# Performance work log

Measured on AMD Instinct MI355X. Metric: run time of the kernel, lower is better.

The kernel has to match this reference:

```python
import jax, jax.numpy as jnp
import numpy as np

D = 64        # emb_size
L = 4         # n_layers
ND = 4        # directions per layer: v2c, c2v, v2k, k2v
N_VAR, N_CONS, N_CUT = 100000, 50000, 20000
E_VC, E_VK = 800000, 200000
EF = 8        # edge feature dim
LN_EPS = 1e-3  # keras LayerNormalization default epsilon


def mlp2(x, w1, b1, w2, b2):
    # Dense(relu) -> Dense(linear); dropout is identity (training=False)
    return jax.nn.relu(x @ w1 + b1) @ w2 + b2


def layer_norm(x, g, b):
    m = jnp.mean(x, axis=-1, keepdims=True)
    v = jnp.var(x, axis=-1, keepdims=True)
    return (x - m) * jax.lax.rsqrt(v + LN_EPS) * g + b


def message_pass(node, neigh, src, dst, ew, P, i):
    """One MessagePassingLayer. P is a tuple of stacked [16,...] params, i the layer index."""
    (mw1, mb1, mw2, mb2, gw, gb, uw1, ub1, uw2, ub2, lg, lb) = P
    msg = mlp2(neigh, mw1[i], mb1[i], mw2[i], mb2[i])          # [N_src, D]
    wm = msg[src] * ew                                          # [E, D] gather + weight
    n = node.shape[0]
    agg = jax.ops.segment_sum(wm, dst, num_segments=n)          # scatter_nd sum
    deg = jax.ops.segment_sum(ew, dst, num_segments=n)          # [n, 1]
    agg = agg / jnp.maximum(deg, 1.0)
    comb = jnp.concatenate([agg, node], axis=-1)                # [n, 2D]
    gate = jax.nn.sigmoid(comb @ gw[i] + gb[i])
    upd = mlp2(comb, uw1[i], ub1[i], uw2[i], ub2[i])
    out = gate * upd + (1.0 - gate) * node
    return layer_norm(out, lg[i], lb[i])


def edge_weight(src_f, dst_f, e_f, w1, b1, w2, b2):
    comb = jnp.concatenate([src_f, dst_f, e_f], axis=-1)
    return jax.nn.sigmoid(jax.nn.relu(comb @ w1 + b1) @ w2 + b2)  # [E, 1]


def setup_inputs() -> dict:
    keys = iter(jax.random.split(jax.random.key(0), 64))

    def p(shape, scale=0.05):
        return jax.random.normal(next(keys), shape, dtype=jnp.float32) * scale

    inp = {
        'variable_features': jax.random.normal(next(keys), (N_VAR, 19), dtype=jnp.float32),
        'constraint_features': jax.random.normal(next(keys), (N_CONS, 5), dtype=jnp.float32),
        'cut_features': jax.random.normal(next(keys), (N_CUT, 30), dtype=jnp.float32),
        'var_cons_edge_features': jax.random.normal(next(keys), (E_VC, EF), dtype=jnp.float32),
        'var_cut_edge_features': jax.random.normal(next(keys), (E_VK, EF), dtype=jnp.float32),
        'var_cons_edges': jnp.stack([
            jax.random.randint(next(keys), (E_VC,), 0, N_VAR, dtype=jnp.int32),
            jax.random.randint(next(keys), (E_VC,), 0, N_CONS, dtype=jnp.int32)]),
        'var_cut_edges': jnp.stack([
            jax.random.randint(next(keys), (E_VK,), 0, N_VAR, dtype=jnp.int32),
            jax.random.randint(next(keys), (E_VK,), 0, N_CUT, dtype=jnp.int32)]),
    }
    # embedding MLPs
    for name, din in [('var', 19), ('cons', 5), ('cut', 30)]:
        inp[f'{name}_w1'] = p((din, D)); inp[f'{name}_b1'] = p((D,))
        inp[f'{name}_w2'] = p((D, D));  inp[f'{name}_b2'] = p((D,))
    # edge weight modules (input 2D + edge_feat)
    for name in ['ewvc', 'ewvk']:
        inp[f'{name}_w1'] = p((2 * D + EF, D)); inp[f'{name}_b1'] = p((D,))
        inp[f'{name}_w2'] = p((D, 1));          inp[f'{name}_b2'] = p((1,))
    # 16 message passing layers, stacked; index = layer*4 + direction(v2c,c2v,v2k,k2v)
    NL = L * ND
    inp['mp_msg_w1'] = p((NL, D, D));  inp['mp_msg_b1'] = p((NL, D))
    inp['mp_msg_w2'] = p((NL, D, D));  inp['mp_msg_b2'] = p((NL, D))
    inp['mp_gate_w'] = p((NL, 2 * D, D)); inp['mp_gate_b'] = p((NL, D))
    inp['mp_upd_w1'] = p((NL, 2 * D, D)); inp['mp_upd_b1'] = p((NL, D))
    inp['mp_upd_w2'] = p((NL, D, D));  inp['mp_upd_b2'] = p((NL, D))
    inp['mp_ln_g'] = jnp.ones((NL, D), dtype=jnp.float32)
    inp['mp_ln_b'] = jnp.zeros((NL, D), dtype=jnp.float32)
    return inp


def reference(variable_features, constraint_features, cut_features,
              var_cons_edge_features, var_cut_edge_features,
              var_w1, var_b1, var_w2, var_b2,
              cons_w1, cons_b1, cons_w2, cons_b2,
              cut_w1, cut_b1, cut_w2, cut_b2,
              ewvc_w1, ewvc_b1, ewvc_w2, ewvc_b2,
              ewvk_w1, ewvk_b1, ewvk_w2, ewvk_b2,
              mp_msg_w1, mp_msg_b1, mp_msg_w2, mp_msg_b2,
              mp_gate_w, mp_gate_b, mp_upd_w1, mp_upd_b1,
              mp_upd_w2, mp_upd_b2, mp_ln_g, mp_ln_b,
              var_cons_edges, var_cut_edges):
    h_var = mlp2(variable_features, var_w1, var_b1, var_w2, var_b2)
    h_cons = mlp2(constraint_features, cons_w1, cons_b1, cons_w2, cons_b2)
    h_cut = mlp2(cut_features, cut_w1, cut_b1, cut_w2, cut_b2)

    vc_s, vc_d = var_cons_edges[0], var_cons_edges[1]
    vk_s, vk_d = var_cut_edges[0], var_cut_edges[1]

    vc_w = edge_weight(h_var[vc_s], h_cons[vc_d], var_cons_edge_features,
                       ewvc_w1, ewvc_b1, ewvc_w2, ewvc_b2)
    vk_w = edge_weight(h_var[vk_s], h_cut[vk_d], var_cut_edge_features,
                       ewvk_w1, ewvk_b1, ewvk_w2, ewvk_b2)

    P = (mp_msg_w1, mp_msg_b1, mp_msg_w2, mp_msg_b2, mp_gate_w, mp_gate_b,
         mp_upd_w1, mp_upd_b1, mp_upd_w2, mp_upd_b2, mp_ln_g, mp_ln_b)

    for l in range(L):
        h_cons = message_pass(h_cons, h_var, vc_s, vc_d, vc_w, P, l * ND + 0)
        h_var = message_pass(h_var, h_cons, vc_d, vc_s, vc_w, P, l * ND + 1)  # reverse
        h_cut = message_pass(h_cut, h_var, vk_s, vk_d, vk_w, P, l * ND + 2)
        h_var = message_pass(h_var, h_cut, vk_d, vk_s, vk_w, P, l * ND + 3)  # reverse
    return h_cut
```

## Files before the change

kernel.cpp:

```cpp
#include <hip/hip_runtime.h>

#define DEVINL static __device__ __forceinline__

namespace {

typedef __attribute__((ext_vector_type(8))) short bf16x8;
typedef __attribute__((ext_vector_type(4))) float f32x4;

constexpr int NV = 100000;
constexpr int NC = 50000;
constexpr int NK = 20000;
constexpr int EVC = 800000;
constexpr int EVK = 200000;
constexpr int E_TOT2 = 2 * (EVC + EVK);
constexpr int R_TOT = NC + NV + NK + NV;
constexpr int SCAN_CHUNK = 2048;
constexpr int SCAN_NB = (R_TOT + SCAN_CHUNK - 1) / SCAN_CHUNK;
constexpr int PACK_PER_LAYER = 28672;
constexpr float WQ_SCALE = 16383.0f;
constexpr float WQ_INV = 1.0f / 16383.0f;

__constant__ int c_bin_hi[8] = {12500, 25000, 37500, 50000,
                                83334, 116667, 150000, 270000};
__constant__ int c_seg_lo[8] = {0, 0, 0, 0, EVC, EVC, EVC, 2 * EVC};
__constant__ int c_seg_hi[8] = {EVC, EVC, EVC, EVC,
                                2 * EVC, 2 * EVC, 2 * EVC, E_TOT2};

constexpr int PE_VAR_W1 = 0;
constexpr int PE_VAR_W2 = 2048;
constexpr int PE_CONS_W1 = 6144;
constexpr int PE_CONS_W2 = 8192;
constexpr int PE_CUT_W1 = 12288;
constexpr int PE_CUT_W2 = 14336;
constexpr int PE_EWVC_A = 18432;
constexpr int PE_EWVC_B = 22528;
constexpr int PE_EWVK_A = 26624;
constexpr int PE_EWVK_B = 30720;
constexpr int PE_TOTAL = 34816;

DEVINL unsigned short f2bf(float f) {
  unsigned u = __float_as_uint(f);
  u = u + 0x7fffu + ((u >> 16) & 1u);
  return (unsigned short)(u >> 16);
}
DEVINL float bf2f(unsigned short h) {
  return __uint_as_float((unsigned)h << 16);
}

DEVINL float sigmoid_f(float x) { return 1.0f / (1.0f + __expf(-x)); }

DEVINL void pack_mat(const float* __restrict__ src, int K, int Kpad,
                     unsigned short* __restrict__ dst, int tid) {
  const int ntup = (Kpad / 32) * 256;
  for (int tup = tid; tup < ntup; tup += 256) {
    const int lane = tup & 63;
    const int t = (tup >> 6) & 3;
    const int kb = tup >> 8;
    const int c = t * 16 + (lane & 15);
    const int k0 = kb * 32 + (lane >> 4) * 8;
#pragma unroll
    for (int jj = 0; jj < 8; ++jj)
      dst[tup * 8 + jj] =
          (k0 + jj < K) ? f2bf(src[(k0 + jj) * 64 + c]) : (unsigned short)0;
  }
}

__global__ void __launch_bounds__(256) pack_k(
    const float* __restrict__ mW1, const float* __restrict__ mW2,
    const float* __restrict__ gW, const float* __restrict__ uW1,
    const float* __restrict__ uW2, unsigned short* __restrict__ PW) {
  const int layer = blockIdx.x;
  unsigned short* out = PW + (size_t)layer * PACK_PER_LAYER;
  pack_mat(mW1 + (size_t)layer * 4096, 64, 64, out, threadIdx.x);
  pack_mat(mW2 + (size_t)layer * 4096, 64, 64, out + 4096, threadIdx.x);
  pack_mat(gW + (size_t)layer * 8192, 128, 128, out + 8192, threadIdx.x);
  pack_mat(uW1 + (size_t)layer * 8192, 128, 128, out + 16384, threadIdx.x);
  pack_mat(uW2 + (size_t)layer * 4096, 64, 64, out + 24576, threadIdx.x);
}

__global__ void __launch_bounds__(256) pack_emb_k(
    const float* __restrict__ var_w1, const float* __restrict__ var_w2,
    const float* __restrict__ cons_w1, const float* __restrict__ cons_w2,
    const float* __restrict__ cut_w1, const float* __restrict__ cut_w2,
    const float* __restrict__ ewvc_w1, const float* __restrict__ ewvk_w1,
    unsigned short* __restrict__ P) {
  switch (blockIdx.x) {
    case 0: pack_mat(var_w1, 19, 32, P + PE_VAR_W1, threadIdx.x); break;
    case 1: pack_mat(var_w2, 64, 64, P + PE_VAR_W2, threadIdx.x); break;
    case 2: pack_mat(cons_w1, 5, 32, P + PE_CONS_W1, threadIdx.x); break;
    case 3: pack_mat(cons_w2, 64, 64, P + PE_CONS_W2, threadIdx.x); break;
    case 4: pack_mat(cut_w1, 30, 32, P + PE_CUT_W1, threadIdx.x); break;
    case 5: pack_mat(cut_w2, 64, 64, P + PE_CUT_W2, threadIdx.x); break;
    case 6: pack_mat(ewvc_w1, 64, 64, P + PE_EWVC_A, threadIdx.x); break;
    case 7: pack_mat(ewvc_w1 + 64 * 64, 64, 64, P + PE_EWVC_B, threadIdx.x); break;
    case 8: pack_mat(ewvk_w1, 64, 64, P + PE_EWVK_A, threadIdx.x); break;
    case 9: pack_mat(ewvk_w1 + 64 * 64, 64, 64, P + PE_EWVK_B, threadIdx.x); break;
  }
}

template <int DIN>
__global__ void __launch_bounds__(256) emb_mfma_k(
    const float* __restrict__ X, const unsigned short* __restrict__ W1p_,
    const unsigned short* __restrict__ W2p_, const float* __restrict__ B1,
    const float* __restrict__ B2, unsigned short* __restrict__ OUTb, int N) {
  __shared__ unsigned short lds[4][16 * 72];
  const int wave = threadIdx.x >> 6, l = threadIdx.x & 63;
  const int col = l & 15, quad = l >> 4;
  const int n0_raw = blockIdx.x * 64 + wave * 16;
  const bool dead = n0_raw >= N;
  const int n0 = dead ? 0 : n0_raw;

  bf16x8 a0;
#pragma unroll
  for (int j = 0; j < 8; ++j) {
    const int k = quad * 8 + j;
    a0[j] = (k < DIN) ? (short)f2bf(X[(size_t)(n0 + col) * DIN + k]) : (short)0;
  }
  const bf16x8* W1p = (const bf16x8*)W1p_;
  const bf16x8* W2p = (const bf16x8*)W2p_;
  f32x4 acc[4];
#pragma unroll
  for (int t = 0; t < 4; ++t) {
    const float b = B1[col + 16 * t];
    acc[t] = f32x4{b, b, b, b};
  }
#pragma unroll
  for (int t = 0; t < 4; ++t)
    acc[t] = __builtin_amdgcn_mfma_f32_16x16x32_bf16(a0, W1p[t * 64 + l], acc[t], 0, 0, 0);
  unsigned short* ld = lds[wave];
#pragma unroll
  for (int t = 0; t < 4; ++t)
#pragma unroll
    for (int r = 0; r < 4; ++r)
      ld[(quad * 4 + r) * 72 + col + 16 * t] = f2bf(fmaxf(acc[t][r], 0.0f));
  __syncthreads();
  const bf16x8 h0 = *(const bf16x8*)&ld[col * 72 + quad * 8];
  const bf16x8 h1 = *(const bf16x8*)&ld[col * 72 + 32 + quad * 8];
  f32x4 o[4];
#pragma unroll
  for (int t = 0; t < 4; ++t) {
    const float b = B2[col + 16 * t];
    o[t] = f32x4{b, b, b, b};
  }
#pragma unroll
  for (int t = 0; t < 4; ++t) {
    o[t] = __builtin_amdgcn_mfma_f32_16x16x32_bf16(h0, W2p[t * 64 + l], o[t], 0, 0, 0);
    o[t] = __builtin_amdgcn_mfma_f32_16x16x32_bf16(h1, W2p[(4 + t) * 64 + l], o[t], 0, 0, 0);
  }
  __syncthreads();
#pragma unroll
  for (int t = 0; t < 4; ++t)
#pragma unroll
    for (int r = 0; r < 4; ++r)
      ld[(quad * 4 + r) * 72 + col + 16 * t] = f2bf(o[t][r]);
  __syncthreads();
  if (!dead) {
#pragma unroll
    for (int cc = 0; cc < 2; ++cc) {
      const bf16x8 v = *(const bf16x8*)&ld[col * 72 + (quad * 2 + cc) * 8];
      *(bf16x8*)(OUTb + (size_t)(n0 + col) * 64 + (quad * 2 + cc) * 8) = v;
    }
  }
}

template <int NOUT>
__global__ void __launch_bounds__(256) gemv_mfma_k(
    const unsigned short* __restrict__ Xb, const unsigned short* __restrict__ WpA_,
    const unsigned short* __restrict__ WpB_, const float* __restrict__ Bias,
    unsigned short* __restrict__ OUT0, unsigned short* __restrict__ OUT1, int N) {
  __shared__ unsigned short lds[4][16 * 72];
  const int wave = threadIdx.x >> 6, l = threadIdx.x & 63;
  const int col = l & 15, quad = l >> 4;
  const int n0_raw = blockIdx.x * 64 + wave * 16;
  const bool dead = n0_raw >= N;
  const int n0 = dead ? 0 : n0_raw;
  const unsigned short* xrow = Xb + (size_t)(n0 + col) * 64 + quad * 8;
  const bf16x8 a0 = *(const bf16x8*)xrow;
  const bf16x8 a1 = *(const bf16x8*)(xrow + 32);
  unsigned short* ld = lds[wave];
#pragma unroll
  for (int m = 0; m < NOUT; ++m) {
    const bf16x8* Wp = (const bf16x8*)(m == 0 ? WpA_ : WpB_);
    unsigned short* OUT = (m == 0) ? OUT0 : OUT1;
    f32x4 acc[4];
#pragma unroll
    for (int t = 0; t < 4; ++t) {
      const float b = (Bias != nullptr) ? Bias[col + 16 * t] : 0.0f;
      acc[t] = f32x4{b, b, b, b};
    }
#pragma unroll
    for (int t = 0; t < 4; ++t) {
      acc[t] = __builtin_amdgcn_mfma_f32_16x16x32_bf16(a0, Wp[t * 64 + l], acc[t], 0, 0, 0);
      acc[t] = __builtin_amdgcn_mfma_f32_16x16x32_bf16(a1, Wp[(4 + t) * 64 + l], acc[t], 0, 0, 0);
    }
    if (m > 0) __syncthreads();
#pragma unroll
    for (int t = 0; t < 4; ++t)
#pragma unroll
      for (int r = 0; r < 4; ++r)
        ld[(quad * 4 + r) * 72 + col + 16 * t] = f2bf(acc[t][r]);
    __syncthreads();
    if (!dead) {
#pragma unroll
      for (int cc = 0; cc < 2; ++cc) {
        const bf16x8 v = *(const bf16x8*)&ld[col * 72 + (quad * 2 + cc) * 8];
        *(bf16x8*)(OUT + (size_t)(n0 + col) * 64 + (quad * 2 + cc) * 8) = v;
      }
    }
  }
}

__global__ void __launch_bounds__(256) msg_mfma_k(
    const unsigned short* __restrict__ Xb, const unsigned short* __restrict__ Wp,
    const float* __restrict__ B1, const float* __restrict__ B2,
    unsigned short* __restrict__ MSGb, int N) {
  __shared__ unsigned short lds[4][16 * 72];
  const int wave = threadIdx.x >> 6, l = threadIdx.x & 63;
  const int col = l & 15, quad = l >> 4;
  const int n0_raw = blockIdx.x * 64 + wave * 16;
  const bool dead = n0_raw >= N;
  const int n0 = dead ? 0 : n0_raw;

  const unsigned short* xrow = Xb + (size_t)(n0 + col) * 64 + quad * 8;
  const bf16x8 a0 = *(const bf16x8*)xrow;
  const bf16x8 a1 = *(const bf16x8*)(xrow + 32);
  const bf16x8* W1p = (const bf16x8*)Wp;
  const bf16x8* W2p = (const bf16x8*)(Wp + 4096);

  f32x4 acc[4];
#pragma unroll
  for (int t = 0; t < 4; ++t) {
    const float b = B1[col + 16 * t];
    acc[t] = f32x4{b, b, b, b};
  }
#pragma unroll
  for (int t = 0; t < 4; ++t) {
    acc[t] = __builtin_amdgcn_mfma_f32_16x16x32_bf16(a0, W1p[t * 64 + l], acc[t], 0, 0, 0);
    acc[t] = __builtin_amdgcn_mfma_f32_16x16x32_bf16(a1, W1p[(4 + t) * 64 + l], acc[t], 0, 0, 0);
  }
  unsigned short* ld = lds[wave];
#pragma unroll
  for (int t = 0; t < 4; ++t)
#pragma unroll
    for (int r = 0; r < 4; ++r)
      ld[(quad * 4 + r) * 72 + col + 16 * t] = f2bf(fmaxf(acc[t][r], 0.0f));
  __syncthreads();
  const bf16x8 h0 = *(const bf16x8*)&ld[col * 72 + quad * 8];
  const bf16x8 h1 = *(const bf16x8*)&ld[col * 72 + 32 + quad * 8];
  f32x4 o[4];
#pragma unroll
  for (int t = 0; t < 4; ++t) {
    const float b = B2[col + 16 * t];
    o[t] = f32x4{b, b, b, b};
  }
#pragma unroll
  for (int t = 0; t < 4; ++t) {
    o[t] = __builtin_amdgcn_mfma_f32_16x16x32_bf16(h0, W2p[t * 64 + l], o[t], 0, 0, 0);
    o[t] = __builtin_amdgcn_mfma_f32_16x16x32_bf16(h1, W2p[(4 + t) * 64 + l], o[t], 0, 0, 0);
  }
  __syncthreads();
#pragma unroll
  for (int t = 0; t < 4; ++t)
#pragma unroll
    for (int r = 0; r < 4; ++r)
      ld[(quad * 4 + r) * 72 + col + 16 * t] = f2bf(o[t][r]);
  __syncthreads();
  if (!dead) {
#pragma unroll
    for (int cc = 0; cc < 2; ++cc) {
      const bf16x8 v = *(const bf16x8*)&ld[col * 72 + (quad * 2 + cc) * 8];
      *(bf16x8*)(MSGb + (size_t)(n0 + col) * 64 + (quad * 2 + cc) * 8) = v;
    }
  }
}

template <int WITH_MSG>
__global__ void __launch_bounds__(256) pass_mfma_k(
    const int* __restrict__ row_ptr, const unsigned* __restrict__ adj,
    const float* __restrict__ degi, const unsigned short* __restrict__ MSGsrc,
    const unsigned short* __restrict__ NODEb,
    const unsigned short* __restrict__ gWp, const unsigned short* __restrict__ uW1p,
    const unsigned short* __restrict__ uW2p, const float* __restrict__ gB,
    const float* __restrict__ uB1, const float* __restrict__ uB2,
    const float* __restrict__ LNG, const float* __restrict__ LNB,
    const unsigned short* __restrict__ mWp,
    const float* __restrict__ mB1, const float* __restrict__ mB2,
    float* __restrict__ OUTf, unsigned short* __restrict__ OUTb,
    unsigned short* __restrict__ MSGdst, int base, int N) {
  __shared__ unsigned short lds[4][16 * 72];
  const int wave = threadIdx.x >> 6, l = threadIdx.x & 63;
  const int col = l & 15, quad = l >> 4;
  const int n0_raw = blockIdx.x * 64 + wave * 16;
  const bool dead = n0_raw >= N;
  const int n0 = dead ? 0 : n0_raw;

  const int r = base + n0 + col;
  const int ps = row_ptr[r], pe = row_ptr[r + 1];
  float acc0[8], acc1[8];
#pragma unroll
  for (int j = 0; j < 8; ++j) { acc0[j] = 0.0f; acc1[j] = 0.0f; }
  int p = ps;
  for (; p + 4 <= pe; p += 4) {
    unsigned av[4];
#pragma unroll
    for (int j = 0; j < 4; ++j) av[j] = adj[p + j];
    bf16x8 m0[4], m1[4];
#pragma unroll
    for (int j = 0; j < 4; ++j) {
      const unsigned short* m = MSGsrc + (size_t)(av[j] >> 14) * 64 + quad * 8;
      m0[j] = *(const bf16x8*)m;
      m1[j] = *(const bf16x8*)(m + 32);
    }
#pragma unroll
    for (int j = 0; j < 4; ++j) {
      const float w = (float)(av[j] & 16383u) * WQ_INV;
      const unsigned* u0 = (const unsigned*)&m0[j];
      const unsigned* u1 = (const unsigned*)&m1[j];
#pragma unroll
      for (int q = 0; q < 4; ++q) {
        acc0[2 * q] = fmaf(__uint_as_float(u0[q] << 16), w, acc0[2 * q]);
        acc0[2 * q + 1] = fmaf(__uint_as_float(u0[q] & 0xffff0000u), w, acc0[2 * q + 1]);
        acc1[2 * q] = fmaf(__uint_as_float(u1[q] << 16), w, acc1[2 * q]);
        acc1[2 * q + 1] = fmaf(__uint_as_float(u1[q] & 0xffff0000u), w, acc1[2 * q + 1]);
      }
    }
  }
  for (; p + 2 <= pe; p += 2) {
    const unsigned avA = adj[p], avB = adj[p + 1];
    const unsigned short* mA = MSGsrc + (size_t)(avA >> 14) * 64 + quad * 8;
    const unsigned short* mB = MSGsrc + (size_t)(avB >> 14) * 64 + quad * 8;
    const bf16x8 mA0 = *(const bf16x8*)mA;
    const bf16x8 mA1 = *(const bf16x8*)(mA + 32);
    const bf16x8 mB0 = *(const bf16x8*)mB;
    const bf16x8 mB1v = *(const bf16x8*)(mB + 32);
    const float wA = (float)(avA & 16383u) * WQ_INV;
    const float wB = (float)(avB & 16383u) * WQ_INV;
    const unsigned* uA0 = (const unsigned*)&mA0;
    const unsigned* uA1 = (const unsigned*)&mA1;
    const unsigned* uB0 = (const unsigned*)&mB0;
    const unsigned* uB1v = (const unsigned*)&mB1v;
#pragma unroll
    for (int q = 0; q < 4; ++q) {
      acc0[2 * q] = fmaf(__uint_as_float(uA0[q] << 16), wA, acc0[2 * q]);
      acc0[2 * q + 1] = fmaf(__uint_as_float(uA0[q] & 0xffff0000u), wA, acc0[2 * q + 1]);
      acc1[2 * q] = fmaf(__uint_as_float(uA1[q] << 16), wA, acc1[2 * q]);
      acc1[2 * q + 1] = fmaf(__uint_as_float(uA1[q] & 0xffff0000u), wA, acc1[2 * q + 1]);
      acc0[2 * q] = fmaf(__uint_as_float(uB0[q] << 16), wB, acc0[2 * q]);
      acc0[2 * q + 1] = fmaf(__uint_as_float(uB0[q] & 0xffff0000u), wB, acc0[2 * q + 1]);
      acc1[2 * q] = fmaf(__uint_as_float(uB1v[q] << 16), wB, acc1[2 * q]);
      acc1[2 * q + 1] = fmaf(__uint_as_float(uB1v[q] & 0xffff0000u), wB, acc1[2 * q + 1]);
    }
  }
  if (p < pe) {
    const unsigned av = adj[p];
    const unsigned short* m = MSGsrc + (size_t)(av >> 14) * 64 + quad * 8;
    const bf16x8 m0 = *(const bf16x8*)m;
    const bf16x8 m1 = *(const bf16x8*)(m + 32);
    const float w = (float)(av & 16383u) * WQ_INV;
    const unsigned* u0 = (const unsigned*)&m0;
    const unsigned* u1 = (const unsigned*)&m1;
#pragma unroll
    for (int q = 0; q < 4; ++q) {
      acc0[2 * q] = fmaf(__uint_as_float(u0[q] << 16), w, acc0[2 * q]);
      acc0[2 * q + 1] = fmaf(__uint_as_float(u0[q] & 0xffff0000u), w, acc0[2 * q + 1]);
      acc1[2 * q] = fmaf(__uint_as_float(u1[q] << 16), w, acc1[2 * q]);
      acc1[2 * q + 1] = fmaf(__uint_as_float(u1[q] & 0xffff0000u), w, acc1[2 * q + 1]);
    }
  }
  const float di = degi[r];
  bf16x8 aA0, aA1;
#pragma unroll
  for (int j = 0; j < 8; ++j) {
    aA0[j] = (short)f2bf(acc0[j] * di);
    aA1[j] = (short)f2bf(acc1[j] * di);
  }

  const unsigned short* nrow = NODEb + (size_t)(n0 + col) * 64 + quad * 8;
  const bf16x8 aN0 = *(const bf16x8*)nrow;
  const bf16x8 aN1 = *(const bf16x8*)(nrow + 32);
  const bf16x8* gW = (const bf16x8*)gWp;
  const bf16x8* uW1 = (const bf16x8*)uW1p;
  const bf16x8* uW2 = (const bf16x8*)uW2p;

  f32x4 g[4], u[4];
#pragma unroll
  for (int t = 0; t < 4; ++t) {
    const float bg = gB[col + 16 * t], bu = uB1[col + 16 * t];
    g[t] = f32x4{bg, bg, bg, bg};
    u[t] = f32x4{bu, bu, bu, bu};
  }
#pragma unroll
  for (int t = 0; t < 4; ++t) {
    g[t] = __builtin_amdgcn_mfma_f32_16x16x32_bf16(aA0, gW[t * 64 + l], g[t], 0, 0, 0);
    g[t] = __builtin_amdgcn_mfma_f32_16x16x32_bf16(aA1, gW[(4 + t) * 64 + l], g[t], 0, 0, 0);
    g[t] = __builtin_amdgcn_mfma_f32_16x16x32_bf16(aN0, gW[(8 + t) * 64 + l], g[t], 0, 0, 0);
    g[t] = __builtin_amdgcn_mfma_f32_16x16x32_bf16(aN1, gW[(12 + t) * 64 + l], g[t], 0, 0, 0);
    u[t] = __builtin_amdgcn_mfma_f32_16x16x32_bf16(aA0, uW1[t * 64 + l], u[t], 0, 0, 0);
    u[t] = __builtin_amdgcn_mfma_f32_16x16x32_bf16(aA1, uW1[(4 + t) * 64 + l], u[t], 0, 0, 0);
    u[t] = __builtin_amdgcn_mfma_f32_16x16x32_bf16(aN0, uW1[(8 + t) * 64 + l], u[t], 0, 0, 0);
    u[t] = __builtin_amdgcn_mfma_f32_16x16x32_bf16(aN1, uW1[(12 + t) * 64 + l], u[t], 0, 0, 0);
  }
#pragma unroll
  for (int t = 0; t < 4; ++t)
#pragma unroll
    for (int r2 = 0; r2 < 4; ++r2) g[t][r2] = sigmoid_f(g[t][r2]);

  unsigned short* ld = lds[wave];
#pragma unroll
  for (int t = 0; t < 4; ++t)
#pragma unroll
    for (int r2 = 0; r2 < 4; ++r2)
      ld[(quad * 4 + r2) * 72 + col + 16 * t] = f2bf(fmaxf(u[t][r2], 0.0f));
  const bf16x8 h0 = *(const bf16x8*)&ld[col * 72 + quad * 8];
  const bf16x8 h1 = *(const bf16x8*)&ld[col * 72 + 32 + quad * 8];
  f32x4 o[4];
#pragma unroll
  for (int t = 0; t < 4; ++t) {
    const float b = uB2[col + 16 * t];
    o[t] = f32x4{b, b, b, b};
  }
#pragma unroll
  for (int t = 0; t < 4; ++t) {
    o[t] = __builtin_amdgcn_mfma_f32_16x16x32_bf16(h0, uW2[t * 64 + l], o[t], 0, 0, 0);
    o[t] = __builtin_amdgcn_mfma_f32_16x16x32_bf16(h1, uW2[(4 + t) * 64 + l], o[t], 0, 0, 0);
  }
  float om[4][4];
#pragma unroll
  for (int t = 0; t < 4; ++t)
#pragma unroll
    for (int r2 = 0; r2 < 4; ++r2) {
      const float nd =
          bf2f(NODEb[(size_t)(n0 + quad * 4 + r2) * 64 + col + 16 * t]);
      om[t][r2] = fmaf(g[t][r2], o[t][r2] - nd, nd);
    }
  float outv[4][4];
#pragma unroll
  for (int r2 = 0; r2 < 4; ++r2) {
    float s1 = (om[0][r2] + om[1][r2]) + (om[2][r2] + om[3][r2]);
    float s2 = fmaf(om[0][r2], om[0][r2], fmaf(om[1][r2], om[1][r2],
                fmaf(om[2][r2], om[2][r2], om[3][r2] * om[3][r2])));
#pragma unroll
    for (int off = 1; off < 16; off <<= 1) {
      s1 += __shfl_xor(s1, off, 64);
      s2 += __shfl_xor(s2, off, 64);
    }
    const float m = s1 * (1.0f / 64.0f);
    const float var = s2 * (1.0f / 64.0f) - m * m;
    const float rr = rsqrtf(var + 1e-3f);
#pragma unroll
    for (int t = 0; t < 4; ++t)
      outv[t][r2] = fmaf((om[t][r2] - m) * rr, LNG[col + 16 * t], LNB[col + 16 * t]);
  }
  if (OUTf != nullptr && !dead) {
#pragma unroll
    for (int t = 0; t < 4; ++t)
#pragma unroll
      for (int r2 = 0; r2 < 4; ++r2)
        OUTf[(size_t)(n0 + quad * 4 + r2) * 64 + col + 16 * t] = outv[t][r2];
  }
#pragma unroll
  for (int t = 0; t < 4; ++t)
#pragma unroll
    for (int r2 = 0; r2 < 4; ++r2)
      ld[(quad * 4 + r2) * 72 + col + 16 * t] = f2bf(outv[t][r2]);
  if (OUTb != nullptr && !dead) {
#pragma unroll
    for (int cc = 0; cc < 2; ++cc) {
      const bf16x8 v = *(const bf16x8*)&ld[col * 72 + (quad * 2 + cc) * 8];
      *(bf16x8*)(OUTb + (size_t)(n0 + col) * 64 + (quad * 2 + cc) * 8) = v;
    }
  }

  if constexpr (WITH_MSG) {
    const bf16x8 x0 = *(const bf16x8*)&ld[col * 72 + quad * 8];
    const bf16x8 x1 = *(const bf16x8*)&ld[col * 72 + 32 + quad * 8];
    const bf16x8* W1p = (const bf16x8*)mWp;
    const bf16x8* W2p = (const bf16x8*)(mWp + 4096);
    f32x4 macc[4];
#pragma unroll
    for (int t = 0; t < 4; ++t) {
      const float b = mB1[col + 16 * t];
      macc[t] = f32x4{b, b, b, b};
    }
#pragma unroll
    for (int t = 0; t < 4; ++t) {
      macc[t] = __builtin_amdgcn_mfma_f32_16x16x32_bf16(x0, W1p[t * 64 + l], macc[t], 0, 0, 0);
      macc[t] = __builtin_amdgcn_mfma_f32_16x16x32_bf16(x1, W1p[(4 + t) * 64 + l], macc[t], 0, 0, 0);
    }
#pragma unroll
    for (int t = 0; t < 4; ++t)
#pragma unroll
      for (int r2 = 0; r2 < 4; ++r2)
        ld[(quad * 4 + r2) * 72 + col + 16 * t] = f2bf(fmaxf(macc[t][r2], 0.0f));
    const bf16x8 mh0 = *(const bf16x8*)&ld[col * 72 + quad * 8];
    const bf16x8 mh1 = *(const bf16x8*)&ld[col * 72 + 32 + quad * 8];
    f32x4 mo[4];
#pragma unroll
    for (int t = 0; t < 4; ++t) {
      const float b = mB2[col + 16 * t];
      mo[t] = f32x4{b, b, b, b};
    }
#pragma unroll
    for (int t = 0; t < 4; ++t) {
      mo[t] = __builtin_amdgcn_mfma_f32_16x16x32_bf16(mh0, W2p[t * 64 + l], mo[t], 0, 0, 0);
      mo[t] = __builtin_amdgcn_mfma_f32_16x16x32_bf16(mh1, W2p[(4 + t) * 64 + l], mo[t], 0, 0, 0);
    }
#pragma unroll
    for (int t = 0; t < 4; ++t)
#pragma unroll
      for (int r2 = 0; r2 < 4; ++r2)
        ld[(quad * 4 + r2) * 72 + col + 16 * t] = f2bf(mo[t][r2]);
    if (!dead) {
#pragma unroll
      for (int cc = 0; cc < 2; ++cc) {
        const bf16x8 v = *(const bf16x8*)&ld[col * 72 + (quad * 2 + cc) * 8];
        *(bf16x8*)(MSGdst + (size_t)(n0 + col) * 64 + (quad * 2 + cc) * 8) = v;
      }
    }
  }
}

__global__ void __launch_bounds__(256) edgew_k(
    const int* __restrict__ S, const int* __restrict__ D,
    const float* __restrict__ EFX, const unsigned short* __restrict__ PA,
    const unsigned short* __restrict__ PB, const float* __restrict__ W1C,
    const float* __restrict__ W2, const float* __restrict__ B2,
    unsigned long long* __restrict__ stagedD,
    unsigned long long* __restrict__ stagedS,
    int* __restrict__ counts, int baseD, int baseS, int E) {
  const int l = threadIdx.x & 63;
  const int g = l >> 3, c = l & 7;
  float wc[8][8];
#pragma unroll
  for (int i = 0; i < 8; ++i) {
    const float4 v0 = *(const float4*)(W1C + i * 64 + c * 8);
    const float4 v1 = *(const float4*)(W1C + i * 64 + c * 8 + 4);
    wc[i][0] = v0.x; wc[i][1] = v0.y; wc[i][2] = v0.z; wc[i][3] = v0.w;
    wc[i][4] = v1.x; wc[i][5] = v1.y; wc[i][6] = v1.z; wc[i][7] = v1.w;
  }
  float w2c[8];
  {
    const float4 a0 = *(const float4*)(W2 + c * 8);
    const float4 a1 = *(const float4*)(W2 + c * 8 + 4);
    w2c[0] = a0.x; w2c[1] = a0.y; w2c[2] = a0.z; w2c[3] = a0.w;
    w2c[4] = a1.x; w2c[5] = a1.y; w2c[6] = a1.z; w2c[7] = a1.w;
  }
  const float b2 = B2[0];
  const int wave_id = blockIdx.x * 4 + (threadIdx.x >> 6);
  const int nwaves = gridDim.x * 4;
  for (int t0 = wave_id * 8; t0 < E; t0 += nwaves * 8) {
    const int e = t0 + g;
    const bool ok = e < E;
    const int ee = ok ? e : E - 1;
    const int s = __builtin_nontemporal_load(S + ee);
    const int d = __builtin_nontemporal_load(D + ee);
    int kd = 0, ks = 0;
    const int rd = baseD + d, rs = baseS + s;
    if (ok && c == 0) {
      kd = atomicAdd(&counts[rd], 1);
      ks = atomicAdd(&counts[rs], 1);
    }
    const bf16x8 pa = *(const bf16x8*)(PA + (size_t)s * 64 + c * 8);
    const bf16x8 pb = *(const bf16x8*)(PB + (size_t)d * 64 + c * 8);
    const f32x4 ef0 =
        __builtin_nontemporal_load((const f32x4*)(EFX + (size_t)ee * 8));
    const f32x4 ef1 =
        __builtin_nontemporal_load((const f32x4*)(EFX + (size_t)ee * 8 + 4));
    const unsigned* pau = (const unsigned*)&pa;
    const unsigned* pbu = (const unsigned*)&pb;
    float h[8];
#pragma unroll
    for (int q = 0; q < 4; ++q) {
      h[2 * q] = __uint_as_float(pau[q] << 16) + __uint_as_float(pbu[q] << 16);
      h[2 * q + 1] = __uint_as_float(pau[q] & 0xffff0000u) +
                     __uint_as_float(pbu[q] & 0xffff0000u);
    }
    const float ef[8] = {ef0[0], ef0[1], ef0[2], ef0[3],
                         ef1[0], ef1[1], ef1[2], ef1[3]};
#pragma unroll
    for (int i = 0; i < 8; ++i)
#pragma unroll
      for (int j = 0; j < 8; ++j) h[j] = fmaf(ef[i], wc[i][j], h[j]);
    float t = 0.0f;
#pragma unroll
    for (int j = 0; j < 8; ++j) t = fmaf(fmaxf(h[j], 0.0f), w2c[j], t);
#pragma unroll
    for (int off = 1; off < 8; off <<= 1) t += __shfl_xor(t, off, 64);
    if (ok && c == 0) {
      const float w = sigmoid_f(t + b2);
      const unsigned w14 = (unsigned)(w * WQ_SCALE + 0.5f);
      stagedD[e] =
          (unsigned long long)((unsigned)rd | ((unsigned)kd << 19)) |
          ((unsigned long long)(((unsigned)s << 14) | w14) << 32);
      stagedS[e] =
          (unsigned long long)((unsigned)rs | ((unsigned)ks << 19)) |
          ((unsigned long long)(((unsigned)d << 14) | w14) << 32);
    }
  }
}

__global__ void __launch_bounds__(256) fill_staged_k(
    const unsigned long long* __restrict__ staged,
    const int* __restrict__ row_ptr, unsigned* __restrict__ adj) {
  const int bin = blockIdx.x & 7;
  const int blk = blockIdx.x >> 3;
  const int nblk = gridDim.x >> 3;
  const int lo = (bin == 0) ? 0 : c_bin_hi[bin - 1];
  const int hi = c_bin_hi[bin];
  const int slo = c_seg_lo[bin], shi = c_seg_hi[bin];
  for (int i = slo + blk * 256 + threadIdx.x; i < shi; i += nblk * 256) {
    const unsigned long long v = __builtin_nontemporal_load(staged + i);
    const int row = (int)(v & 0x7ffffull);
    if (row >= lo && row < hi) {
      const int k = (int)((v >> 19) & 0x1fffull);
      adj[row_ptr[row] + k] = (unsigned)(v >> 32);
    }
  }
}

__global__ void __launch_bounds__(256) degi_k(const int* __restrict__ row_ptr,
                                             const unsigned* __restrict__ adj,
                                             float* __restrict__ degi) {
  const int r = blockIdx.x * 256 + threadIdx.x;
  if (r >= R_TOT) return;
  const int s = row_ptr[r], e = row_ptr[r + 1];
  float d = 0.0f;
  for (int p = s; p < e; ++p) d += (float)(adj[p] & 16383u) * WQ_INV;
  degi[r] = 1.0f / fmaxf(d, 1.0f);
}

__global__ void __launch_bounds__(256) scan1_k(const int* __restrict__ in,
                                               int* __restrict__ bsum) {
  __shared__ int sd[256];
  const int t = threadIdx.x;
  const int base = blockIdx.x * SCAN_CHUNK + t * 8;
  int s = 0;
#pragma unroll
  for (int i = 0; i < 8; ++i) {
    const int idx = base + i;
    s += (idx < R_TOT) ? in[idx] : 0;
  }
  sd[t] = s;
  __syncthreads();
  for (int off = 128; off > 0; off >>= 1) {
    if (t < off) sd[t] += sd[t + off];
    __syncthreads();
  }
  if (t == 0) bsum[blockIdx.x] = sd[0];
}

__global__ void __launch_bounds__(256) scan2_k(int* __restrict__ bsum,
                                               int* __restrict__ row_ptr) {
  __shared__ int sd[256];
  const int t = threadIdx.x;
  const int v = (t < SCAN_NB) ? bsum[t] : 0;
  sd[t] = v;
  __syncthreads();
  for (int off = 1; off < 256; off <<= 1) {
    const int add = (t >= off) ? sd[t - off] : 0;
    __syncthreads();
    sd[t] += add;
    __syncthreads();
  }
  if (t < SCAN_NB) bsum[t] = sd[t] - v;
  if (t == 255) row_ptr[R_TOT] = sd[255];
}

__global__ void __launch_bounds__(256) scan3_k(const int* __restrict__ in,
                                               const int* __restrict__ bsum,
                                               int* __restrict__ out) {
  __shared__ int sd[256];
  const int t = threadIdx.x;
  const int base = blockIdx.x * SCAN_CHUNK + t * 8;
  int loc[8];
  int s = 0;
#pragma unroll
  for (int i = 0; i < 8; ++i) {
    loc[i] = s;
    const int idx = base + i;
    s += (idx < R_TOT) ? in[idx] : 0;
  }
  sd[t] = s;
  __syncthreads();
  const int v = s;
  for (int off = 1; off < 256; off <<= 1) {
    const int add = (t >= off) ? sd[t - off] : 0;
    __syncthreads();
    sd[t] += add;
    __syncthreads();
  }
  const int off0 = bsum[blockIdx.x] + (sd[t] - v);
#pragma unroll
  for (int i = 0; i < 8; ++i) {
    const int idx = base + i;
    if (idx < R_TOT) out[idx] = off0 + loc[i];
  }
}

}

extern "C" void kernel_launch(void* const* d_in, const int* in_sizes, int n_in,
                              void* d_out, int out_size, void* d_ws, size_t ws_size,
                              hipStream_t stream) {
  (void)in_sizes; (void)n_in; (void)out_size; (void)ws_size;

  const float* variable_features   = (const float*)d_in[0];
  const float* constraint_features = (const float*)d_in[1];
  const float* cut_features        = (const float*)d_in[2];
  const float* vc_ef = (const float*)d_in[3];
  const float* vk_ef = (const float*)d_in[4];
  const int* vc_edges = (const int*)d_in[5];
  const int* vk_edges = (const int*)d_in[6];
  const int *vc_s = vc_edges, *vc_d = vc_edges + EVC;
  const int *vk_s = vk_edges, *vk_d = vk_edges + EVK;
  const float* var_w1  = (const float*)d_in[7];
  const float* var_b1  = (const float*)d_in[8];
  const float* var_w2  = (const float*)d_in[9];
  const float* var_b2  = (const float*)d_in[10];
  const float* cons_w1 = (const float*)d_in[11];
  const float* cons_b1 = (const float*)d_in[12];
  const float* cons_w2 = (const float*)d_in[13];
  const float* cons_b2 = (const float*)d_in[14];
  const float* cut_w1  = (const float*)d_in[15];
  const float* cut_b1  = (const float*)d_in[16];
  const float* cut_w2  = (const float*)d_in[17];
  const float* cut_b2  = (const float*)d_in[18];
  const float* ewvc_w1 = (const float*)d_in[19];
  const float* ewvc_b1 = (const float*)d_in[20];
  const float* ewvc_w2 = (const float*)d_in[21];
  const float* ewvc_b2 = (const float*)d_in[22];
  const float* ewvk_w1 = (const float*)d_in[23];
  const float* ewvk_b1 = (const float*)d_in[24];
  const float* ewvk_w2 = (const float*)d_in[25];
  const float* ewvk_b2 = (const float*)d_in[26];
  const float* mp_msg_w1 = (const float*)d_in[27];
  const float* mp_msg_b1 = (const float*)d_in[28];
  const float* mp_msg_w2 = (const float*)d_in[29];
  const float* mp_msg_b2 = (const float*)d_in[30];
  const float* mp_gate_w = (const float*)d_in[31];
  const float* mp_gate_b = (const float*)d_in[32];
  const float* mp_upd_w1 = (const float*)d_in[33];
  const float* mp_upd_b1 = (const float*)d_in[34];
  const float* mp_upd_w2 = (const float*)d_in[35];
  const float* mp_upd_b2 = (const float*)d_in[36];
  const float* mp_ln_g   = (const float*)d_in[37];
  const float* mp_ln_b   = (const float*)d_in[38];

  char* wp = (char*)d_ws;
  auto take = [&](size_t nbytes) {
    char* p = wp;
    wp += (nbytes + 255) & ~(size_t)255;
    return p;
  };
  unsigned short* h_var_b  = (unsigned short*)take((size_t)NV * 64 * 2);
  unsigned short* h_cons_b = (unsigned short*)take((size_t)NC * 64 * 2);
  unsigned short* h_cut_b  = (unsigned short*)take((size_t)NK * 64 * 2);
  unsigned short* msg_ping = (unsigned short*)take((size_t)NV * 64 * 2);
  unsigned short* msg_pong = (unsigned short*)take((size_t)NV * 64 * 2);
  unsigned short* pa = (unsigned short*)take((size_t)NV * 64 * 2);
  unsigned short* pb = (unsigned short*)take((size_t)NC * 64 * 2);
  unsigned short* qa = (unsigned short*)take((size_t)NV * 64 * 2);
  unsigned short* qb = (unsigned short*)take((size_t)NK * 64 * 2);
  unsigned short* packW = (unsigned short*)take((size_t)15 * PACK_PER_LAYER * 2);
  unsigned short* packE = (unsigned short*)take((size_t)PE_TOTAL * 2);
  int* row_ptr = (int*)take((size_t)(R_TOT + 1) * 4);
  int* counts  = (int*)take((size_t)R_TOT * 4);
  int* bsum    = (int*)take(256 * 4);
  float* degi  = (float*)take((size_t)R_TOT * 4);
  unsigned* adj = (unsigned*)take((size_t)(2 * EVC + 2 * EVK) * 4);

  unsigned long long* staged = (unsigned long long*)msg_ping;

  hipMemsetAsync(counts, 0, (size_t)R_TOT * 4, stream);

  pack_k<<<15, 256, 0, stream>>>(mp_msg_w1, mp_msg_w2, mp_gate_w, mp_upd_w1,
                                 mp_upd_w2, packW);
  pack_emb_k<<<10, 256, 0, stream>>>(var_w1, var_w2, cons_w1, cons_w2, cut_w1,
                                     cut_w2, ewvc_w1, ewvk_w1, packE);

  emb_mfma_k<19><<<(NV + 63) / 64, 256, 0, stream>>>(
      variable_features, packE + PE_VAR_W1, packE + PE_VAR_W2, var_b1, var_b2,
      h_var_b, NV);
  emb_mfma_k<5><<<(NC + 63) / 64, 256, 0, stream>>>(
      constraint_features, packE + PE_CONS_W1, packE + PE_CONS_W2, cons_b1,
      cons_b2, h_cons_b, NC);
  emb_mfma_k<30><<<(NK + 63) / 64, 256, 0, stream>>>(
      cut_features, packE + PE_CUT_W1, packE + PE_CUT_W2, cut_b1, cut_b2,
      h_cut_b, NK);

  gemv_mfma_k<2><<<(NV + 63) / 64, 256, 0, stream>>>(
      h_var_b, packE + PE_EWVC_A, packE + PE_EWVK_A, nullptr, pa, qa, NV);
  gemv_mfma_k<1><<<(NC + 63) / 64, 256, 0, stream>>>(
      h_cons_b, packE + PE_EWVC_B, nullptr, ewvc_b1, pb, nullptr, NC);
  gemv_mfma_k<1><<<(NK + 63) / 64, 256, 0, stream>>>(
      h_cut_b, packE + PE_EWVK_B, nullptr, ewvk_b1, qb, nullptr, NK);

  edgew_k<<<1024, 256, 0, stream>>>(vc_s, vc_d, vc_ef, pa, pb,
                                    ewvc_w1 + 128 * 64, ewvc_w2, ewvc_b2,
                                    staged, staged + EVC, counts, 0, NC, EVC);
  edgew_k<<<512, 256, 0, stream>>>(vk_s, vk_d, vk_ef, qa, qb,
                                   ewvk_w1 + 128 * 64, ewvk_w2, ewvk_b2,
                                   staged + 2 * EVC, staged + 2 * EVC + EVK,
                                   counts, NC + NV, NC + NV + NK, EVK);

  scan1_k<<<SCAN_NB, 256, 0, stream>>>(counts, bsum);
  scan2_k<<<1, 256, 0, stream>>>(bsum, row_ptr);
  scan3_k<<<SCAN_NB, 256, 0, stream>>>(counts, bsum, row_ptr);
  fill_staged_k<<<8 * 192, 256, 0, stream>>>(staged, row_ptr, adj);
  degi_k<<<(R_TOT + 255) / 256, 256, 0, stream>>>(row_ptr, adj, degi);

  unsigned short* nodeb_t[4] = {h_cons_b, h_var_b, h_cut_b, h_var_b};
  const int Nd_t[4] = {NC, NV, NK, NV};
  const int base_t[4] = {0, NC, NC + NV, NC + NV + NK};

  msg_mfma_k<<<(NV + 63) / 64, 256, 0, stream>>>(
      h_var_b, packW, mp_msg_b1, mp_msg_b2, msg_ping, NV);

  for (int i = 0; i < 15; ++i) {
    const int d = i & 3;
    const int Nd = Nd_t[d], base = base_t[d];
    const unsigned short* Wl = packW + (size_t)i * PACK_PER_LAYER;
    const unsigned short* src = (i % 2 == 0) ? msg_ping : msg_pong;
    unsigned short* dst = (i % 2 == 0) ? msg_pong : msg_ping;

    if (i < 14) {
      const unsigned short* Wn = packW + (size_t)(i + 1) * PACK_PER_LAYER;
      pass_mfma_k<1><<<(Nd + 63) / 64, 256, 0, stream>>>(
          row_ptr, adj, degi, src, nodeb_t[d], Wl + 8192, Wl + 16384,
          Wl + 24576, mp_gate_b + (size_t)i * 64, mp_upd_b1 + (size_t)i * 64,
          mp_upd_b2 + (size_t)i * 64, mp_ln_g + (size_t)i * 64,
          mp_ln_b + (size_t)i * 64, Wn, mp_msg_b1 + (size_t)(i + 1) * 64,
          mp_msg_b2 + (size_t)(i + 1) * 64, nullptr, nodeb_t[d], dst, base, Nd);
    } else {
      pass_mfma_k<0><<<(Nd + 63) / 64, 256, 0, stream>>>(
          row_ptr, adj, degi, src, nodeb_t[d], Wl + 8192, Wl + 16384,
          Wl + 24576, mp_gate_b + (size_t)i * 64, mp_upd_b1 + (size_t)i * 64,
          mp_upd_b2 + (size_t)i * 64, mp_ln_g + (size_t)i * 64,
          mp_ln_b + (size_t)i * 64, nullptr, nullptr, nullptr,
          (float*)d_out, nullptr, nullptr, base, Nd);
    }
  }
}
```

Before: 800.3 us.

## Merge embedding, gemv and edge-weight launches; compute degree inline in pass

```diff
diff --git a/kernel.cpp b/kernel.cpp
--- a/kernel.cpp
+++ b/kernel.cpp
@@ -19,6 +19,11 @@
 constexpr int PACK_PER_LAYER = 28672;
 constexpr float WQ_SCALE = 16383.0f;
 constexpr float WQ_INV = 1.0f / 16383.0f;
+
+constexpr int NB_EVC = 1024, NB_EVK = 512;
+constexpr int NB_VAR = (NV + 63) / 64;
+constexpr int NB_CONS = (NC + 63) / 64;
+constexpr int NB_CUT = (NK + 63) / 64;
 
 __constant__ int c_bin_hi[8] = {12500, 25000, 37500, 50000,
                                 83334, 116667, 150000, 270000};
@@ -99,14 +104,16 @@
 }
 
 template <int DIN>
-__global__ void __launch_bounds__(256) emb_mfma_k(
-    const float* __restrict__ X, const unsigned short* __restrict__ W1p_,
-    const unsigned short* __restrict__ W2p_, const float* __restrict__ B1,
-    const float* __restrict__ B2, unsigned short* __restrict__ OUTb, int N) {
-  __shared__ unsigned short lds[4][16 * 72];
-  const int wave = threadIdx.x >> 6, l = threadIdx.x & 63;
+DEVINL void emb_body(const float* __restrict__ X,
+                     const unsigned short* __restrict__ W1p_,
+                     const unsigned short* __restrict__ W2p_,
+                     const float* __restrict__ B1, const float* __restrict__ B2,
+                     unsigned short* __restrict__ OUTb, int N, int bid,
+                     unsigned short* __restrict__ ld) {
+  const int l = threadIdx.x & 63;
+  const int wave = threadIdx.x >> 6;
   const int col = l & 15, quad = l >> 4;
-  const int n0_raw = blockIdx.x * 64 + wave * 16;
+  const int n0_raw = bid * 64 + wave * 16;
   const bool dead = n0_raw >= N;
   const int n0 = dead ? 0 : n0_raw;
 
@@ -127,13 +134,11 @@
 #pragma unroll
   for (int t = 0; t < 4; ++t)
     acc[t] = __builtin_amdgcn_mfma_f32_16x16x32_bf16(a0, W1p[t * 64 + l], acc[t], 0, 0, 0);
-  unsigned short* ld = lds[wave];
 #pragma unroll
   for (int t = 0; t < 4; ++t)
 #pragma unroll
     for (int r = 0; r < 4; ++r)
       ld[(quad * 4 + r) * 72 + col + 16 * t] = f2bf(fmaxf(acc[t][r], 0.0f));
-  __syncthreads();
   const bf16x8 h0 = *(const bf16x8*)&ld[col * 72 + quad * 8];
   const bf16x8 h1 = *(const bf16x8*)&ld[col * 72 + 32 + quad * 8];
   f32x4 o[4];
@@ -147,13 +152,11 @@
     o[t] = __builtin_amdgcn_mfma_f32_16x16x32_bf16(h0, W2p[t * 64 + l], o[t], 0, 0, 0);
     o[t] = __builtin_amdgcn_mfma_f32_16x16x32_bf16(h1, W2p[(4 + t) * 64 + l], o[t], 0, 0, 0);
   }
-  __syncthreads();
 #pragma unroll
   for (int t = 0; t < 4; ++t)
 #pragma unroll
     for (int r = 0; r < 4; ++r)
       ld[(quad * 4 + r) * 72 + col + 16 * t] = f2bf(o[t][r]);
-  __syncthreads();
   if (!dead) {
 #pragma unroll
     for (int cc = 0; cc < 2; ++cc) {
@@ -163,21 +166,44 @@
   }
 }
 
+__global__ void __launch_bounds__(256) emb3_k(
+    const float* __restrict__ Xv, const float* __restrict__ Xc,
+    const float* __restrict__ Xk, const unsigned short* __restrict__ P,
+    const float* __restrict__ vB1, const float* __restrict__ vB2,
+    const float* __restrict__ cB1, const float* __restrict__ cB2,
+    const float* __restrict__ kB1, const float* __restrict__ kB2,
+    unsigned short* __restrict__ Ov, unsigned short* __restrict__ Oc,
+    unsigned short* __restrict__ Ok) {
+  __shared__ unsigned short lds[4][16 * 72];
+  unsigned short* ld = lds[threadIdx.x >> 6];
+  const int b = blockIdx.x;
+  if (b < NB_VAR)
+    emb_body<19>(Xv, P + PE_VAR_W1, P + PE_VAR_W2, vB1, vB2, Ov, NV, b, ld);
+  else if (b < NB_VAR + NB_CONS)
+    emb_body<5>(Xc, P + PE_CONS_W1, P + PE_CONS_W2, cB1, cB2, Oc, NC,
+                b - NB_VAR, ld);
+  else
+    emb_body<30>(Xk, P + PE_CUT_W1, P + PE_CUT_W2, kB1, kB2, Ok, NK,
+                 b - NB_VAR - NB_CONS, ld);
+}
+
 template <int NOUT>
-__global__ void __launch_bounds__(256) gemv_mfma_k(
-    const unsigned short* __restrict__ Xb, const unsigned short* __restrict__ WpA_,
-    const unsigned short* __restrict__ WpB_, const float* __restrict__ Bias,
-    unsigned short* __restrict__ OUT0, unsigned short* __restrict__ OUT1, int N) {
-  __shared__ unsigned short lds[4][16 * 72];
-  const int wave = threadIdx.x >> 6, l = threadIdx.x & 63;
+DEVINL void gemv_body(const unsigned short* __restrict__ Xb,
+                      const unsigned short* __restrict__ WpA_,
+                      const unsigned short* __restrict__ WpB_,
+                      const float* __restrict__ Bias,
+                      unsigned short* __restrict__ OUT0,
+                      unsigned short* __restrict__ OUT1, int N, int bid,
+                      unsigned short* __restrict__ ld) {
+  const int l = threadIdx.x & 63;
+  const int wave = threadIdx.x >> 6;
   const int col = l & 15, quad = l >> 4;
-  const int n0_raw = blockIdx.x * 64 + wave * 16;
+  const int n0_raw = bid * 64 + wave * 16;
   const bool dead = n0_raw >= N;
   const int n0 = dead ? 0 : n0_raw;
   const unsigned short* xrow = Xb + (size_t)(n0 + col) * 64 + quad * 8;
   const bf16x8 a0 = *(const bf16x8*)xrow;
   const bf16x8 a1 = *(const bf16x8*)(xrow + 32);
-  unsigned short* ld = lds[wave];
 #pragma unroll
   for (int m = 0; m < NOUT; ++m) {
     const bf16x8* Wp = (const bf16x8*)(m == 0 ? WpA_ : WpB_);
@@ -193,13 +219,11 @@
       acc[t] = __builtin_amdgcn_mfma_f32_16x16x32_bf16(a0, Wp[t * 64 + l], acc[t], 0, 0, 0);
       acc[t] = __builtin_amdgcn_mfma_f32_16x16x32_bf16(a1, Wp[(4 + t) * 64 + l], acc[t], 0, 0, 0);
     }
-    if (m > 0) __syncthreads();
 #pragma unroll
     for (int t = 0; t < 4; ++t)
 #pragma unroll
       for (int r = 0; r < 4; ++r)
         ld[(quad * 4 + r) * 72 + col + 16 * t] = f2bf(acc[t][r]);
-    __syncthreads();
     if (!dead) {
 #pragma unroll
       for (int cc = 0; cc < 2; ++cc) {
@@ -208,6 +232,27 @@
       }
     }
   }
+}
+
+__global__ void __launch_bounds__(256) gemv3_k(
+    const unsigned short* __restrict__ h_var,
+    const unsigned short* __restrict__ h_cons,
+    const unsigned short* __restrict__ h_cut,
+    const unsigned short* __restrict__ P, const float* __restrict__ cBias,
+    const float* __restrict__ kBias, unsigned short* __restrict__ pa,
+    unsigned short* __restrict__ qa, unsigned short* __restrict__ pb,
+    unsigned short* __restrict__ qb) {
+  __shared__ unsigned short lds[4][16 * 72];
+  unsigned short* ld = lds[threadIdx.x >> 6];
+  const int b = blockIdx.x;
+  if (b < NB_VAR)
+    gemv_body<2>(h_var, P + PE_EWVC_A, P + PE_EWVK_A, nullptr, pa, qa, NV, b, ld);
+  else if (b < NB_VAR + NB_CONS)
+    gemv_body<1>(h_cons, P + PE_EWVC_B, nullptr, cBias, pb, nullptr, NC,
+                 b - NB_VAR, ld);
+  else
+    gemv_body<1>(h_cut, P + PE_EWVK_B, nullptr, kBias, qb, nullptr, NK,
+                 b - NB_VAR - NB_CONS, ld);
 }
 
 __global__ void __launch_bounds__(256) msg_mfma_k(
@@ -244,7 +289,6 @@
 #pragma unroll
     for (int r = 0; r < 4; ++r)
       ld[(quad * 4 + r) * 72 + col + 16 * t] = f2bf(fmaxf(acc[t][r], 0.0f));
-  __syncthreads();
   const bf16x8 h0 = *(const bf16x8*)&ld[col * 72 + quad * 8];
   const bf16x8 h1 = *(const bf16x8*)&ld[col * 72 + 32 + quad * 8];
   f32x4 o[4];
@@ -258,13 +302,11 @@
     o[t] = __builtin_amdgcn_mfma_f32_16x16x32_bf16(h0, W2p[t * 64 + l], o[t], 0, 0, 0);
     o[t] = __builtin_amdgcn_mfma_f32_16x16x32_bf16(h1, W2p[(4 + t) * 64 + l], o[t], 0, 0, 0);
   }
-  __syncthreads();
 #pragma unroll
   for (int t = 0; t < 4; ++t)
 #pragma unroll
     for (int r = 0; r < 4; ++r)
       ld[(quad * 4 + r) * 72 + col + 16 * t] = f2bf(o[t][r]);
-  __syncthreads();
   if (!dead) {
 #pragma unroll
     for (int cc = 0; cc < 2; ++cc) {
@@ -277,7 +319,7 @@
 template <int WITH_MSG>
 __global__ void __launch_bounds__(256) pass_mfma_k(
     const int* __restrict__ row_ptr, const unsigned* __restrict__ adj,
-    const float* __restrict__ degi, const unsigned short* __restrict__ MSGsrc,
+    const unsigned short* __restrict__ MSGsrc,
     const unsigned short* __restrict__ NODEb,
     const unsigned short* __restrict__ gWp, const unsigned short* __restrict__ uW1p,
     const unsigned short* __restrict__ uW2p, const float* __restrict__ gB,
@@ -299,6 +341,7 @@
   float acc0[8], acc1[8];
 #pragma unroll
   for (int j = 0; j < 8; ++j) { acc0[j] = 0.0f; acc1[j] = 0.0f; }
+  float wsum = 0.0f;
   int p = ps;
   for (; p + 4 <= pe; p += 4) {
     unsigned av[4];
@@ -314,6 +357,7 @@
 #pragma unroll
     for (int j = 0; j < 4; ++j) {
       const float w = (float)(av[j] & 16383u) * WQ_INV;
+      wsum += w;
       const unsigned* u0 = (const unsigned*)&m0[j];
       const unsigned* u1 = (const unsigned*)&m1[j];
 #pragma unroll
@@ -335,6 +379,8 @@
     const bf16x8 mB1v = *(const bf16x8*)(mB + 32);
     const float wA = (float)(avA & 16383u) * WQ_INV;
     const float wB = (float)(avB & 16383u) * WQ_INV;
+    wsum += wA;
+    wsum += wB;
     const unsigned* uA0 = (const unsigned*)&mA0;
     const unsigned* uA1 = (const unsigned*)&mA1;
     const unsigned* uB0 = (const unsigned*)&mB0;
@@ -357,6 +403,7 @@
     const bf16x8 m0 = *(const bf16x8*)m;
     const bf16x8 m1 = *(const bf16x8*)(m + 32);
     const float w = (float)(av & 16383u) * WQ_INV;
+    wsum += w;
     const unsigned* u0 = (const unsigned*)&m0;
     const unsigned* u1 = (const unsigned*)&m1;
 #pragma unroll
@@ -367,7 +414,7 @@
       acc1[2 * q + 1] = fmaf(__uint_as_float(u1[q] & 0xffff0000u), w, acc1[2 * q + 1]);
     }
   }
-  const float di = degi[r];
+  const float di = 1.0f / fmaxf(wsum, 1.0f);
   bf16x8 aA0, aA1;
 #pragma unroll
   for (int j = 0; j < 8; ++j) {
@@ -520,14 +567,16 @@
   }
 }
 
-__global__ void __launch_bounds__(256) edgew_k(
-    const int* __restrict__ S, const int* __restrict__ D,
-    const float* __restrict__ EFX, const unsigned short* __restrict__ PA,
-    const unsigned short* __restrict__ PB, const float* __restrict__ W1C,
-    const float* __restrict__ W2, const float* __restrict__ B2,
-    unsigned long long* __restrict__ stagedD,
-    unsigned long long* __restrict__ stagedS,
-    int* __restrict__ counts, int baseD, int baseS, int E) {
+DEVINL void edgew_body(const int* __restrict__ S, const int* __restrict__ D,
+                       const float* __restrict__ EFX,
+                       const unsigned short* __restrict__ PA,
+                       const unsigned short* __restrict__ PB,
+                       const float* __restrict__ W1C,
+                       const float* __restrict__ W2, const float* __restrict__ B2,
+                       unsigned long long* __restrict__ stagedD,
+                       unsigned long long* __restrict__ stagedS,
+                       int* __restrict__ counts, int baseD, int baseS, int E,
+                       int bid, int nb) {
   const int l = threadIdx.x & 63;
   const int g = l >> 3, c = l & 7;
   float wc[8][8];
@@ -546,8 +595,8 @@
     w2c[4] = a1.x; w2c[5] = a1.y; w2c[6] = a1.z; w2c[7] = a1.w;
   }
   const float b2 = B2[0];
-  const int wave_id = blockIdx.x * 4 + (threadIdx.x >> 6);
-  const int nwaves = gridDim.x * 4;
+  const int wave_id = bid * 4 + (threadIdx.x >> 6);
+  const int nwaves = nb * 4;
   for (int t0 = wave_id * 8; t0 < E; t0 += nwaves * 8) {
     const int e = t0 + g;
     const bool ok = e < E;
@@ -597,6 +646,26 @@
           ((unsigned long long)(((unsigned)d << 14) | w14) << 32);
     }
   }
+}
+
+__global__ void __launch_bounds__(256) edgew2_k(
+    const int* __restrict__ S0, const int* __restrict__ D0,
+    const float* __restrict__ EFX0, const unsigned short* __restrict__ PA0,
+    const unsigned short* __restrict__ PB0, const float* __restrict__ W1C0,
+    const float* __restrict__ W20, const float* __restrict__ B20,
+    unsigned long long* __restrict__ sD0, unsigned long long* __restrict__ sS0,
+    const int* __restrict__ S1, const int* __restrict__ D1,
+    const float* __restrict__ EFX1, const unsigned short* __restrict__ PA1,
+    const unsigned short* __restrict__ PB1, const float* __restrict__ W1C1,
+    const float* __restrict__ W21, const float* __restrict__ B21,
+    unsigned long long* __restrict__ sD1, unsigned long long* __restrict__ sS1,
+    int* __restrict__ counts) {
+  if (blockIdx.x < NB_EVC)
+    edgew_body(S0, D0, EFX0, PA0, PB0, W1C0, W20, B20, sD0, sS0, counts,
+               0, NC, EVC, blockIdx.x, NB_EVC);
+  else
+    edgew_body(S1, D1, EFX1, PA1, PB1, W1C1, W21, B21, sD1, sS1, counts,
+               NC + NV, NC + NV + NK, EVK, blockIdx.x - NB_EVC, NB_EVK);
 }
 
 __global__ void __launch_bounds__(256) fill_staged_k(
@@ -616,17 +685,6 @@
       adj[row_ptr[row] + k] = (unsigned)(v >> 32);
     }
   }
-}
-
-__global__ void __launch_bounds__(256) degi_k(const int* __restrict__ row_ptr,
-                                             const unsigned* __restrict__ adj,
-                                             float* __restrict__ degi) {
-  const int r = blockIdx.x * 256 + threadIdx.x;
-  if (r >= R_TOT) return;
-  const int s = row_ptr[r], e = row_ptr[r + 1];
-  float d = 0.0f;
-  for (int p = s; p < e; ++p) d += (float)(adj[p] & 16383u) * WQ_INV;
-  degi[r] = 1.0f / fmaxf(d, 1.0f);
 }
 
 __global__ void __launch_bounds__(256) scan1_k(const int* __restrict__ in,
@@ -766,7 +824,6 @@
   int* row_ptr = (int*)take((size_t)(R_TOT + 1) * 4);
   int* counts  = (int*)take((size_t)R_TOT * 4);
   int* bsum    = (int*)take(256 * 4);
-  float* degi  = (float*)take((size_t)R_TOT * 4);
   unsigned* adj = (unsigned*)take((size_t)(2 * EVC + 2 * EVK) * 4);
 
   unsigned long long* staged = (unsigned long long*)msg_ping;
@@ -778,36 +835,24 @@
   pack_emb_k<<<10, 256, 0, stream>>>(var_w1, var_w2, cons_w1, cons_w2, cut_w1,
                                      cut_w2, ewvc_w1, ewvk_w1, packE);
 
-  emb_mfma_k<19><<<(NV + 63) / 64, 256, 0, stream>>>(
-      variable_features, packE + PE_VAR_W1, packE + PE_VAR_W2, var_b1, var_b2,
-      h_var_b, NV);
-  emb_mfma_k<5><<<(NC + 63) / 64, 256, 0, stream>>>(
-      constraint_features, packE + PE_CONS_W1, packE + PE_CONS_W2, cons_b1,
-      cons_b2, h_cons_b, NC);
-  emb_mfma_k<30><<<(NK + 63) / 64, 256, 0, stream>>>(
-      cut_features, packE + PE_CUT_W1, packE + PE_CUT_W2, cut_b1, cut_b2,
-      h_cut_b, NK);
-
-  gemv_mfma_k<2><<<(NV + 63) / 64, 256, 0, stream>>>(
-      h_var_b, packE + PE_EWVC_A, packE + PE_EWVK_A, nullptr, pa, qa, NV);
-  gemv_mfma_k<1><<<(NC + 63) / 64, 256, 0, stream>>>(
-      h_cons_b, packE + PE_EWVC_B, nullptr, ewvc_b1, pb, nullptr, NC);
-  gemv_mfma_k<1><<<(NK + 63) / 64, 256, 0, stream>>>(
-      h_cut_b, packE + PE_EWVK_B, nullptr, ewvk_b1, qb, nullptr, NK);
-
-  edgew_k<<<1024, 256, 0, stream>>>(vc_s, vc_d, vc_ef, pa, pb,
-                                    ewvc_w1 + 128 * 64, ewvc_w2, ewvc_b2,
-                                    staged, staged + EVC, counts, 0, NC, EVC);
-  edgew_k<<<512, 256, 0, stream>>>(vk_s, vk_d, vk_ef, qa, qb,
-                                   ewvk_w1 + 128 * 64, ewvk_w2, ewvk_b2,
-                                   staged + 2 * EVC, staged + 2 * EVC + EVK,
-                                   counts, NC + NV, NC + NV + NK, EVK);
+  emb3_k<<<NB_VAR + NB_CONS + NB_CUT, 256, 0, stream>>>(
+      variable_features, constraint_features, cut_features, packE,
+      var_b1, var_b2, cons_b1, cons_b2, cut_b1, cut_b2,
+      h_var_b, h_cons_b, h_cut_b);
+
+  gemv3_k<<<NB_VAR + NB_CONS + NB_CUT, 256, 0, stream>>>(
+      h_var_b, h_cons_b, h_cut_b, packE, ewvc_b1, ewvk_b1, pa, qa, pb, qb);
+
+  edgew2_k<<<NB_EVC + NB_EVK, 256, 0, stream>>>(
+      vc_s, vc_d, vc_ef, pa, pb, ewvc_w1 + 128 * 64, ewvc_w2, ewvc_b2,
+      staged, staged + EVC,
+      vk_s, vk_d, vk_ef, qa, qb, ewvk_w1 + 128 * 64, ewvk_w2, ewvk_b2,
+      staged + 2 * EVC, staged + 2 * EVC + EVK, counts);
 
   scan1_k<<<SCAN_NB, 256, 0, stream>>>(counts, bsum);
   scan2_k<<<1, 256, 0, stream>>>(bsum, row_ptr);
   scan3_k<<<SCAN_NB, 256, 0, stream>>>(counts, bsum, row_ptr);
   fill_staged_k<<<8 * 192, 256, 0, stream>>>(staged, row_ptr, adj);
-  degi_k<<<(R_TOT + 255) / 256, 256, 0, stream>>>(row_ptr, adj, degi);
 
   unsigned short* nodeb_t[4] = {h_cons_b, h_var_b, h_cut_b, h_var_b};
   const int Nd_t[4] = {NC, NV, NK, NV};
@@ -826,14 +871,14 @@
     if (i < 14) {
       const unsigned short* Wn = packW + (size_t)(i + 1) * PACK_PER_LAYER;
       pass_mfma_k<1><<<(Nd + 63) / 64, 256, 0, stream>>>(
-          row_ptr, adj, degi, src, nodeb_t[d], Wl + 8192, Wl + 16384,
+          row_ptr, adj, src, nodeb_t[d], Wl + 8192, Wl + 16384,
           Wl + 24576, mp_gate_b + (size_t)i * 64, mp_upd_b1 + (size_t)i * 64,
           mp_upd_b2 + (size_t)i * 64, mp_ln_g + (size_t)i * 64,
           mp_ln_b + (size_t)i * 64, Wn, mp_msg_b1 + (size_t)(i + 1) * 64,
           mp_msg_b2 + (size_t)(i + 1) * 64, nullptr, nodeb_t[d], dst, base, Nd);
     } else {
       pass_mfma_k<0><<<(Nd + 63) / 64, 256, 0, stream>>>(
-          row_ptr, adj, degi, src, nodeb_t[d], Wl + 8192, Wl + 16384,
+          row_ptr, adj, src, nodeb_t[d], Wl + 8192, Wl + 16384,
           Wl + 24576, mp_gate_b + (size_t)i * 64, mp_upd_b1 + (size_t)i * 64,
           mp_upd_b2 + (size_t)i * 64, mp_ln_g + (size_t)i * 64,
           mp_ln_b + (size_t)i * 64, nullptr, nullptr, nullptr,
```

Result: faster. 775.3 us (median of 2 runs) (-3.1%).
